# Kernel tuning notes

Hardware: AMD Instinct MI355X
Metric: run time of the kernel (lower is better)

Reference implementation:

```python
import jax, jax.numpy as jnp
import numpy as np

HIDDEN = 768
NUM_LABELS = 64


def setup_inputs() -> dict:
    key = jax.random.key(0)
    k1, k2, k3, k4, k5 = jax.random.split(key, 5)
    B, S = 16, 4096
    com_features = jax.random.normal(k1, (B, S, HIDDEN), dtype=jnp.float32)
    labels = jax.random.randint(k2, (B, S), 0, NUM_LABELS + 1, dtype=jnp.int64)
    label_feature = jax.random.normal(k3, (NUM_LABELS, HIDDEN), dtype=jnp.float32)
    # nn.Linear(1536, 768): weight [out, in], bias [out]
    merge_w = jax.random.normal(k4, (HIDDEN, 2 * HIDDEN), dtype=jnp.float32) * (1.0 / np.sqrt(2 * HIDDEN))
    merge_b = jax.random.normal(k5, (HIDDEN,), dtype=jnp.float32) * 0.01
    return {"com_features": com_features, "labels": labels,
            "label_feature": label_feature, "merge_w": merge_w, "merge_b": merge_b}


def reference(com_features, labels, label_feature, merge_w, merge_b):
    B, S, H = com_features.shape
    tokens_emb = com_features.reshape(-1, H)          # [N, H]
    token_labels = labels.reshape(-1)                  # [N]
    active = token_labels != 0                         # label 0 = inactive
    # label_id = label - 1 indexes the concatenated label-feature table.
    # Clip so inactive rows gather a valid (ignored) row; result is masked out.
    label_id = jnp.clip(token_labels - 1, 0, label_feature.shape[0] - 1)
    centers = label_feature[label_id]                  # [N, H] gather
    # merge(cat(token_emb, center)) == token @ W_left^T + center @ W_right^T + b
    cat = jnp.concatenate([tokens_emb, centers], axis=-1)  # [N, 2H]
    merged = cat @ merge_w.T + merge_b                 # [N, H]
    # scatter_ back into token embeddings: active rows replaced by merged.
    out = jnp.where(active[:, None], merged, tokens_emb)
    return out.reshape(B, S, H)
```

## Files before the change

### kernel.cpp

```cpp
#include <hip/hip_runtime.h>
#include <hip/hip_bf16.h>

#define HID 768
#define WROW 1536
#define NLAB 64

typedef __attribute__((ext_vector_type(8))) __bf16 bf16x8;
typedef __attribute__((ext_vector_type(4))) float f32x4;

__device__ __forceinline__ bf16x8 pk8(float4 a, float4 b) {
    return (bf16x8){(__bf16)a.x, (__bf16)a.y, (__bf16)a.z, (__bf16)a.w,
                    (__bf16)b.x, (__bf16)b.y, (__bf16)b.z, (__bf16)b.w};
}

__global__ __launch_bounds__(256) void compute_P_kernel(
    const float* __restrict__ lf,
    const float* __restrict__ W,
    const float* __restrict__ bias,
    float* __restrict__ P)
{
    const int j = blockIdx.x;
    const int t = threadIdx.x;
    __shared__ __align__(16) float wrow[HID];
    if (t < 192)
        *(float4*)(wrow + t * 4) =
            *(const float4*)(W + (size_t)j * WROW + HID + t * 4);
    __syncthreads();

    const int lab = t >> 2;
    const int seg = t & 3;
    const float* lfp = lf + lab * HID + seg * 192;
    const float* wp  = wrow + seg * 192;
    float acc = 0.f;
    #pragma unroll 8
    for (int i = 0; i < 192; i += 4) {
        float4 u = *(const float4*)(lfp + i);
        float4 v = *(const float4*)(wp + i);
        acc += u.x * v.x + u.y * v.y + u.z * v.z + u.w * v.w;
    }
    acc += __shfl_xor(acc, 1);
    acc += __shfl_xor(acc, 2);
    if (seg == 0) P[lab * HID + j] = acc + bias[j];
}

__global__ __launch_bounds__(256) void merge_gemm_kernel(
    const float* __restrict__ A,
    const int* __restrict__ labels,
    const float* __restrict__ W,
    const float* __restrict__ P,
    float* __restrict__ out,
    const int nwg)
{
    __shared__ __align__(16) unsigned short As[2][128 * 32];
    __shared__ __align__(16) unsigned short Bs[2][128 * 32];
    __shared__ int Ls[128];

    int bid = blockIdx.x;
    if ((nwg & 7) == 0) {
        const int q = nwg >> 3;
        bid = (bid & 7) * q + (bid >> 3);
    }
    const int m0 = (bid / (HID / 128)) * 128;
    const int j0 = (bid % (HID / 128)) * 128;

    const int t = threadIdx.x;
    if (t < 128) Ls[t] = labels[m0 + t];

    const int w  = t >> 6;
    const int l  = t & 63;
    const int lm = l & 15;
    const int lk = l >> 4;
    const int qm = (w >> 1) * 64;
    const int qn = (w & 1) * 64;

    const int sr = t >> 2;
    const int sc = t & 3;
    const float* gA  = A + (size_t)(m0 + sr) * HID  + sc * 8;
    const float* gA2 = gA + (size_t)64 * HID;
    const float* gB  = W + (size_t)(j0 + sr) * WROW + sc * 8;
    const float* gB2 = gB + (size_t)64 * WROW;
    const int eoff = sr * 32 + ((sc ^ (sr & 3)) * 8);

    float4 ra0, ra1, ra2, ra3, rb0, rb1, rb2, rb3;
    f32x4 acc[4][4] = {};

#define ISSUE(K) do { \
    ra0 = *(const float4*)(gA  + (K));      ra1 = *(const float4*)(gA  + (K) + 4); \
    ra2 = *(const float4*)(gA2 + (K));      ra3 = *(const float4*)(gA2 + (K) + 4); \
    rb0 = *(const float4*)(gB  + (K));      rb1 = *(const float4*)(gB  + (K) + 4); \
    rb2 = *(const float4*)(gB2 + (K));      rb3 = *(const float4*)(gB2 + (K) + 4); \
} while (0)

    ISSUE(0);
    int p = 0;
    for (int k0 = 0; k0 < HID; k0 += 32) {
        *(bf16x8*)&As[p][eoff]        = pk8(ra0, ra1);
        *(bf16x8*)&As[p][eoff + 2048] = pk8(ra2, ra3);
        *(bf16x8*)&Bs[p][eoff]        = pk8(rb0, rb1);
        *(bf16x8*)&Bs[p][eoff + 2048] = pk8(rb2, rb3);
        if (k0 + 32 < HID) ISSUE(k0 + 32);
        __syncthreads();

        bf16x8 af[4], bfr[4];
        #pragma unroll
        for (int mi = 0; mi < 4; ++mi) {
            const int r = qm + mi * 16 + lm;
            af[mi] = *(const bf16x8*)&As[p][r * 32 + ((lk ^ (r & 3)) * 8)];
        }
        #pragma unroll
        for (int ni = 0; ni < 4; ++ni) {
            const int r = qn + ni * 16 + lm;
            bfr[ni] = *(const bf16x8*)&Bs[p][r * 32 + ((lk ^ (r & 3)) * 8)];
        }

        #pragma unroll
        for (int mi = 0; mi < 4; ++mi)
            #pragma unroll
            for (int ni = 0; ni < 4; ++ni)
                acc[mi][ni] = __builtin_amdgcn_mfma_f32_16x16x32_bf16(
                    af[mi], bfr[ni], acc[mi][ni], 0, 0, 0);

        p ^= 1;
    }
#undef ISSUE

    #pragma unroll
    for (int mi = 0; mi < 4; ++mi) {
        const int rowb = qm + mi * 16 + lk * 4;
        #pragma unroll
        for (int r = 0; r < 4; ++r) {
            const int n_tok = m0 + rowb + r;
            const int lab   = Ls[rowb + r];
            const size_t rowoff = (size_t)n_tok * HID;
            #pragma unroll
            for (int ni = 0; ni < 4; ++ni) {
                const int j = j0 + qn + ni * 16 + lm;
                float v;
                if (lab != 0)
                    v = acc[mi][ni][r] + P[(size_t)(lab - 1) * HID + j];
                else
                    v = A[rowoff + j];
                out[rowoff + j] = v;
            }
        }
    }
}

extern "C" void kernel_launch(void* const* d_in, const int* in_sizes, int n_in,
                              void* d_out, int out_size, void* d_ws, size_t ws_size,
                              hipStream_t stream) {
    const float* com    = (const float*)d_in[0];
    const int*   labels = (const int*)d_in[1];
    const float* lf     = (const float*)d_in[2];
    const float* W      = (const float*)d_in[3];
    const float* bias   = (const float*)d_in[4];
    float* out = (float*)d_out;
    float* P = (float*)d_ws;

    const int n_rows = in_sizes[0] / HID;
    compute_P_kernel<<<dim3(HID), dim3(256), 0, stream>>>(lf, W, bias, P);
    const int nwg = (n_rows / 128) * (HID / 128);
    merge_gemm_kernel<<<dim3(nwg), dim3(256), 0, stream>>>(
        com, labels, W, P, out, nwg);
}
```

Before: 531.0 us.

## Pre-convert activations and weights to bf16 and stage tiles via async global-to-LDS loads

New measurement: 531.2 us. No clear change (+0.0%).

```diff
diff --git a/kernel.cpp b/kernel.cpp
--- a/kernel.cpp
+++ b/kernel.cpp
@@ -11,6 +11,36 @@
 __device__ __forceinline__ bf16x8 pk8(float4 a, float4 b) {
     return (bf16x8){(__bf16)a.x, (__bf16)a.y, (__bf16)a.z, (__bf16)a.w,
                     (__bf16)b.x, (__bf16)b.y, (__bf16)b.z, (__bf16)b.w};
+}
+
+__device__ __forceinline__ void async16(const void* g, void* l) {
+    __builtin_amdgcn_global_load_lds(
+        (const __attribute__((address_space(1))) void*)g,
+        (__attribute__((address_space(3))) void*)l,
+        16, 0, 0);
+}
+
+__global__ __launch_bounds__(256) void cvtA_kernel(
+    const float* __restrict__ src, unsigned short* __restrict__ dst, long n8)
+{
+    long i = (long)blockIdx.x * 256 + threadIdx.x;
+    const long stride = (long)gridDim.x * 256;
+    for (; i < n8; i += stride) {
+        float4 a = *(const float4*)(src + i * 8);
+        float4 b = *(const float4*)(src + i * 8 + 4);
+        *(bf16x8*)(dst + i * 8) = pk8(a, b);
+    }
+}
+
+__global__ __launch_bounds__(256) void cvtW_kernel(
+    const float* __restrict__ W, unsigned short* __restrict__ Wb)
+{
+    const int u = blockIdx.x * 256 + threadIdx.x;
+    const int j = u / 96;
+    const int c = (u % 96) * 8;
+    float4 a = *(const float4*)(W + (size_t)j * WROW + c);
+    float4 b = *(const float4*)(W + (size_t)j * WROW + c + 4);
+    *(bf16x8*)(Wb + (size_t)j * HID + c) = pk8(a, b);
 }
 
 __global__ __launch_bounds__(256) void compute_P_kernel(
@@ -43,10 +73,11 @@
     if (seg == 0) P[lab * HID + j] = acc + bias[j];
 }
 
-__global__ __launch_bounds__(256) void merge_gemm_kernel(
+__global__ __launch_bounds__(256) void merge_gemm_bf16_kernel(
+    const unsigned short* __restrict__ Ab,
     const float* __restrict__ A,
     const int* __restrict__ labels,
-    const float* __restrict__ W,
+    const unsigned short* __restrict__ Wb,
     const float* __restrict__ P,
     float* __restrict__ out,
     const int nwg)
@@ -56,7 +87,7 @@
     __shared__ int Ls[128];
 
     int bid = blockIdx.x;
-    if ((nwg & 7) == 0) {
+    {
         const int q = nwg >> 3;
         bid = (bid & 7) * q + (bid >> 3);
     }
@@ -73,56 +104,46 @@
     const int qm = (w >> 1) * 64;
     const int qn = (w & 1) * 64;
 
-    const int sr = t >> 2;
-    const int sc = t & 3;
-    const float* gA  = A + (size_t)(m0 + sr) * HID  + sc * 8;
-    const float* gA2 = gA + (size_t)64 * HID;
-    const float* gB  = W + (size_t)(j0 + sr) * WROW + sc * 8;
-    const float* gB2 = gB + (size_t)64 * WROW;
-    const int eoff = sr * 32 + ((sc ^ (sr & 3)) * 8);
-
-    float4 ra0, ra1, ra2, ra3, rb0, rb1, rb2, rb3;
+    const unsigned short* gA = Ab + (size_t)(m0 + (t >> 2)) * HID + (t & 3) * 8;
+    const unsigned short* gB = Wb + (size_t)(j0 + (t >> 2)) * HID + (t & 3) * 8;
+
     f32x4 acc[4][4] = {};
 
-#define ISSUE(K) do { \
-    ra0 = *(const float4*)(gA  + (K));      ra1 = *(const float4*)(gA  + (K) + 4); \
-    ra2 = *(const float4*)(gA2 + (K));      ra3 = *(const float4*)(gA2 + (K) + 4); \
-    rb0 = *(const float4*)(gB  + (K));      rb1 = *(const float4*)(gB  + (K) + 4); \
-    rb2 = *(const float4*)(gB2 + (K));      rb3 = *(const float4*)(gB2 + (K) + 4); \
+#define STAGE(buf, K) do { \
+    async16(gA + (K),                    &As[buf][t * 8]);        \
+    async16(gA + (size_t)64 * HID + (K), &As[buf][t * 8 + 2048]); \
+    async16(gB + (K),                    &Bs[buf][t * 8]);        \
+    async16(gB + (size_t)64 * HID + (K), &Bs[buf][t * 8 + 2048]); \
 } while (0)
 
-    ISSUE(0);
-    int p = 0;
-    for (int k0 = 0; k0 < HID; k0 += 32) {
-        *(bf16x8*)&As[p][eoff]        = pk8(ra0, ra1);
-        *(bf16x8*)&As[p][eoff + 2048] = pk8(ra2, ra3);
-        *(bf16x8*)&Bs[p][eoff]        = pk8(rb0, rb1);
-        *(bf16x8*)&Bs[p][eoff + 2048] = pk8(rb2, rb3);
-        if (k0 + 32 < HID) ISSUE(k0 + 32);
+#define COMPUTE(buf) do { \
+    bf16x8 af[4], bfr[4]; \
+    _Pragma("unroll") \
+    for (int mi = 0; mi < 4; ++mi) \
+        af[mi] = *(const bf16x8*)&As[buf][(qm + mi * 16 + lm) * 32 + lk * 8]; \
+    _Pragma("unroll") \
+    for (int ni = 0; ni < 4; ++ni) \
+        bfr[ni] = *(const bf16x8*)&Bs[buf][(qn + ni * 16 + lm) * 32 + lk * 8]; \
+    _Pragma("unroll") \
+    for (int mi = 0; mi < 4; ++mi) \
+        _Pragma("unroll") \
+        for (int ni = 0; ni < 4; ++ni) \
+            acc[mi][ni] = __builtin_amdgcn_mfma_f32_16x16x32_bf16( \
+                af[mi], bfr[ni], acc[mi][ni], 0, 0, 0); \
+} while (0)
+
+    STAGE(0, 0);
+    int cur = 0;
+    __syncthreads();
+    for (int k0 = 32; k0 < HID; k0 += 32) {
+        STAGE(cur ^ 1, k0);
+        COMPUTE(cur);
         __syncthreads();
-
-        bf16x8 af[4], bfr[4];
-        #pragma unroll
-        for (int mi = 0; mi < 4; ++mi) {
-            const int r = qm + mi * 16 + lm;
-            af[mi] = *(const bf16x8*)&As[p][r * 32 + ((lk ^ (r & 3)) * 8)];
-        }
-        #pragma unroll
-        for (int ni = 0; ni < 4; ++ni) {
-            const int r = qn + ni * 16 + lm;
-            bfr[ni] = *(const bf16x8*)&Bs[p][r * 32 + ((lk ^ (r & 3)) * 8)];
-        }
-
-        #pragma unroll
-        for (int mi = 0; mi < 4; ++mi)
-            #pragma unroll
-            for (int ni = 0; ni < 4; ++ni)
-                acc[mi][ni] = __builtin_amdgcn_mfma_f32_16x16x32_bf16(
-                    af[mi], bfr[ni], acc[mi][ni], 0, 0, 0);
-
-        p ^= 1;
-    }
-#undef ISSUE
+        cur ^= 1;
+    }
+    COMPUTE(cur);
+#undef STAGE
+#undef COMPUTE
 
     #pragma unroll
     for (int mi = 0; mi < 4; ++mi) {
@@ -146,6 +167,107 @@
     }
 }
 
+__global__ __launch_bounds__(256) void merge_gemm_kernel(
+    const float* __restrict__ A,
+    const int* __restrict__ labels,
+    const float* __restrict__ W,
+    const float* __restrict__ P,
+    float* __restrict__ out,
+    const int nwg)
+{
+    __shared__ __align__(16) unsigned short As[2][128 * 32];
+    __shared__ __align__(16) unsigned short Bs[2][128 * 32];
+    __shared__ int Ls[128];
+
+    int bid = blockIdx.x;
+    if ((nwg & 7) == 0) {
+        const int q = nwg >> 3;
+        bid = (bid & 7) * q + (bid >> 3);
+    }
+    const int m0 = (bid / (HID / 128)) * 128;
+    const int j0 = (bid % (HID / 128)) * 128;
+
+    const int t = threadIdx.x;
+    if (t < 128) Ls[t] = labels[m0 + t];
+
+    const int w  = t >> 6;
+    const int l  = t & 63;
+    const int lm = l & 15;
+    const int lk = l >> 4;
+    const int qm = (w >> 1) * 64;
+    const int qn = (w & 1) * 64;
+
+    const int sr = t >> 2;
+    const int sc = t & 3;
+    const float* gA  = A + (size_t)(m0 + sr) * HID  + sc * 8;
+    const float* gA2 = gA + (size_t)64 * HID;
+    const float* gB  = W + (size_t)(j0 + sr) * WROW + sc * 8;
+    const float* gB2 = gB + (size_t)64 * WROW;
+    const int eoff = sr * 32 + ((sc ^ (sr & 3)) * 8);
+
+    float4 ra0, ra1, ra2, ra3, rb0, rb1, rb2, rb3;
+    f32x4 acc[4][4] = {};
+
+#define ISSUE(K) do { \
+    ra0 = *(const float4*)(gA  + (K));      ra1 = *(const float4*)(gA  + (K) + 4); \
+    ra2 = *(const float4*)(gA2 + (K));      ra3 = *(const float4*)(gA2 + (K) + 4); \
+    rb0 = *(const float4*)(gB  + (K));      rb1 = *(const float4*)(gB  + (K) + 4); \
+    rb2 = *(const float4*)(gB2 + (K));      rb3 = *(const float4*)(gB2 + (K) + 4); \
+} while (0)
+
+    ISSUE(0);
+    int p = 0;
+    for (int k0 = 0; k0 < HID; k0 += 32) {
+        *(bf16x8*)&As[p][eoff]        = pk8(ra0, ra1);
+        *(bf16x8*)&As[p][eoff + 2048] = pk8(ra2, ra3);
+        *(bf16x8*)&Bs[p][eoff]        = pk8(rb0, rb1);
+        *(bf16x8*)&Bs[p][eoff + 2048] = pk8(rb2, rb3);
+        if (k0 + 32 < HID) ISSUE(k0 + 32);
+        __syncthreads();
+
+        bf16x8 af[4], bfr[4];
+        #pragma unroll
+        for (int mi = 0; mi < 4; ++mi) {
+            const int r = qm + mi * 16 + lm;
+            af[mi] = *(const bf16x8*)&As[p][r * 32 + ((lk ^ (r & 3)) * 8)];
+        }
+        #pragma unroll
+        for (int ni = 0; ni < 4; ++ni) {
+            const int r = qn + ni * 16 + lm;
+            bfr[ni] = *(const bf16x8*)&Bs[p][r * 32 + ((lk ^ (r & 3)) * 8)];
+        }
+        #pragma unroll
+        for (int mi = 0; mi < 4; ++mi)
+            #pragma unroll
+            for (int ni = 0; ni < 4; ++ni)
+                acc[mi][ni] = __builtin_amdgcn_mfma_f32_16x16x32_bf16(
+                    af[mi], bfr[ni], acc[mi][ni], 0, 0, 0);
+        p ^= 1;
+    }
+#undef ISSUE
+
+    #pragma unroll
+    for (int mi = 0; mi < 4; ++mi) {
+        const int rowb = qm + mi * 16 + lk * 4;
+        #pragma unroll
+        for (int r = 0; r < 4; ++r) {
+            const int n_tok = m0 + rowb + r;
+            const int lab   = Ls[rowb + r];
+            const size_t rowoff = (size_t)n_tok * HID;
+            #pragma unroll
+            for (int ni = 0; ni < 4; ++ni) {
+                const int j = j0 + qn + ni * 16 + lm;
+                float v;
+                if (lab != 0)
+                    v = acc[mi][ni][r] + P[(size_t)(lab - 1) * HID + j];
+                else
+                    v = A[rowoff + j];
+                out[rowoff + j] = v;
+            }
+        }
+    }
+}
+
 extern "C" void kernel_launch(void* const* d_in, const int* in_sizes, int n_in,
                               void* d_out, int out_size, void* d_ws, size_t ws_size,
                               hipStream_t stream) {
@@ -155,11 +277,27 @@
     const float* W      = (const float*)d_in[3];
     const float* bias   = (const float*)d_in[4];
     float* out = (float*)d_out;
+
+    const int n_rows = in_sizes[0] / HID;
+    const int nwg = (n_rows / 128) * (HID / 128);
+
     float* P = (float*)d_ws;
-
-    const int n_rows = in_sizes[0] / HID;
-    compute_P_kernel<<<dim3(HID), dim3(256), 0, stream>>>(lf, W, bias, P);
-    const int nwg = (n_rows / 128) * (HID / 128);
-    merge_gemm_kernel<<<dim3(nwg), dim3(256), 0, stream>>>(
-        com, labels, W, P, out, nwg);
-}
+    const size_t off_Wb = (size_t)NLAB * HID * 4;
+    const size_t off_Ab = off_Wb + (size_t)HID * HID * 2;
+    const size_t need   = off_Ab + (size_t)n_rows * HID * 2;
+
+    if (ws_size >= need) {
+        unsigned short* Wb = (unsigned short*)((char*)d_ws + off_Wb);
+        unsigned short* Ab = (unsigned short*)((char*)d_ws + off_Ab);
+        const long n8 = (long)n_rows * HID / 8;
+        cvtA_kernel<<<dim3(2048), dim3(256), 0, stream>>>(com, Ab, n8);
+        cvtW_kernel<<<dim3(HID * 96 / 256), dim3(256), 0, stream>>>(W, Wb);
+        compute_P_kernel<<<dim3(HID), dim3(256), 0, stream>>>(lf, W, bias, P);
+        merge_gemm_bf16_kernel<<<dim3(nwg), dim3(256), 0, stream>>>(
+            Ab, com, labels, Wb, P, out, nwg);
+    } else {
+        compute_P_kernel<<<dim3(HID), dim3(256), 0, stream>>>(lf, W, bias, P);
+        merge_gemm_kernel<<<dim3(nwg), dim3(256), 0, stream>>>(
+            com, labels, W, P, out, nwg);
+    }
+}
```
